# Performance work log

Hardware: AMD Instinct MI355X
Metric: run time of the kernel (lower is better)

The kernel has to match this reference:

```python
import jax, jax.numpy as jnp
import numpy as np

B, T, D_MODEL = 2, 2048, 2048
N_HEAD, N_KV, HD = 32, 8, 64


def _rope_tables(T, hd, base=10000.0):
    # standard rotary tables, (T, hd) with frequencies repeated over both halves
    inv_freq = 1.0 / (base ** (np.arange(0, hd // 2, dtype=np.float32) / (hd // 2)))
    t = np.arange(T, dtype=np.float32)
    freqs = np.outer(t, inv_freq)            # (T, hd/2)
    emb = np.concatenate([freqs, freqs], axis=-1)  # (T, hd)
    return jnp.asarray(np.cos(emb)), jnp.asarray(np.sin(emb))


def setup_inputs() -> dict:
    key = jax.random.key(0)
    ks = jax.random.split(key, 5)
    cos, sin = _rope_tables(T, HD)
    s = 0.02
    return {
        "x": jax.random.normal(ks[0], (B, T, D_MODEL), jnp.float32),
        "cos": cos,
        "sin": sin,
        "Wq": jax.random.normal(ks[1], (N_HEAD * HD, D_MODEL), jnp.float32) * s,
        "Wk": jax.random.normal(ks[2], (N_KV * HD, D_MODEL), jnp.float32) * s,
        "Wv": jax.random.normal(ks[3], (N_KV * HD, D_MODEL), jnp.float32) * s,
        "Wo": jax.random.normal(ks[4], (D_MODEL, N_HEAD * HD), jnp.float32) * s,
    }


def _apply_rope(x, cos, sin):
    # x: (B, H, T, D); cos/sin: (T, D)
    D = x.shape[-1]
    x1, x2 = x[..., : D // 2], x[..., D // 2 :]
    rot = jnp.concatenate([-x2, x1], axis=-1)
    c = cos[: x.shape[-2]][None, None]
    s = sin[: x.shape[-2]][None, None]
    return x * c + rot * s


def reference(x, cos, sin, Wq, Wk, Wv, Wo):
    Bv, Tv, _ = x.shape
    q = (x @ Wq.T).reshape(Bv, Tv, N_HEAD, HD).transpose(0, 2, 1, 3)  # (B,H,T,D)
    k = (x @ Wk.T).reshape(Bv, Tv, N_KV, HD).transpose(0, 2, 1, 3)    # (B,Hkv,T,D)
    v = (x @ Wv.T).reshape(Bv, Tv, N_KV, HD).transpose(0, 2, 1, 3)
    q = _apply_rope(q, cos, sin)
    k = _apply_rope(k, cos, sin)
    repeat = N_HEAD // N_KV
    if repeat > 1:
        k = jnp.repeat(k, repeat, axis=1)
        v = jnp.repeat(v, repeat, axis=1)
    scale = 1.0 / jnp.sqrt(jnp.float32(HD)).astype(x.dtype)
    scores = jnp.einsum("bhqd,bhkd->bhqk", q, k) * scale
    causal = jnp.tril(jnp.ones((Tv, Tv), dtype=bool))
    scores = jnp.where(causal[None, None], scores, jnp.finfo(scores.dtype).min)
    attn = jax.nn.softmax(scores, axis=-1)
    out = jnp.einsum("bhqk,bhkd->bhqd", attn, v)
    out = out.transpose(0, 2, 1, 3).reshape(Bv, Tv, N_HEAD * HD)
    return out @ Wo.T
```

## Files before the change

### kernel.cpp

```cpp
#include <hip/hip_runtime.h>
#include <stdint.h>

#define B_SZ 2
#define T_SEQ 2048
#define DM 2048
#define NH 32
#define NKV 8
#define HD 64
#define QKV_W 3072

typedef unsigned short u16;
typedef __bf16 bf16x8 __attribute__((ext_vector_type(8)));
typedef float floatx4 __attribute__((ext_vector_type(4)));

__device__ __forceinline__ float bf2f(u16 u) {
  union { unsigned u; float f; } v; v.u = ((unsigned)u) << 16; return v.f;
}
__device__ __forceinline__ u16 f2bf(float f) {
  union { float f; unsigned u; } v; v.f = f;
  unsigned r = v.u + 0x7fff + ((v.u >> 16) & 1);
  return (u16)(r >> 16);
}
__device__ __forceinline__ unsigned pk2bf(float hi, float lo) {
  return __builtin_amdgcn_perm(__float_as_uint(hi), __float_as_uint(lo), 0x07060302u);
}
__device__ __forceinline__ float fexp2(float x) {
#if __has_builtin(__builtin_amdgcn_exp2f)
  return __builtin_amdgcn_exp2f(x);
#else
  return exp2f(x);
#endif
}

__device__ __forceinline__ void gld_lds16(const void* g, void* l) {
  __builtin_amdgcn_global_load_lds(
      (const __attribute__((address_space(1))) unsigned int*)g,
      (__attribute__((address_space(3))) unsigned int*)l, 16, 0, 0);
}

__global__ __launch_bounds__(256) void conv_kernel(
    const float* __restrict__ src, u16* __restrict__ dst, int n4)
{
  int i = blockIdx.x * 256 + threadIdx.x;
  int stride = gridDim.x * 256;
  for (; i < n4; i += stride) {
    float4 v = ((const float4*)src)[i];
    ushort4 o;
    o.x = f2bf(v.x); o.y = f2bf(v.y); o.z = f2bf(v.z); o.w = f2bf(v.w);
    ((ushort4*)dst)[i] = o;
  }
}

__global__ __launch_bounds__(256) void gemm_qkv_kernel(
    const u16* __restrict__ A, const u16* __restrict__ Bt,
    u16* __restrict__ C)
{
  __shared__ __align__(16) u16 sA[128 * 32];
  __shared__ __align__(16) u16 sB[128 * 32];

  const int n0 = blockIdx.x * 128;
  const int m0 = blockIdx.y * 128;
  const int K = 2048;

  const int tid  = threadIdx.x;
  const int lane = tid & 63;
  const int w    = tid >> 6;
  const int wm = w >> 1, wn = w & 1;
  const int lm = lane & 15, lq = lane >> 4;

  floatx4 acc[4][4];
  #pragma unroll
  for (int i = 0; i < 4; i++)
    #pragma unroll
    for (int j = 0; j < 4; j++) { floatx4 z = {0.f,0.f,0.f,0.f}; acc[i][j] = z; }

  const int ar = tid >> 2;
  const int ac = (tid & 3) * 8;
  const u16* Ap0 = A  + (size_t)(m0 + ar) * K + ac;
  const u16* Ap1 = A  + (size_t)(m0 + 64 + ar) * K + ac;
  const u16* Bp0 = Bt + (size_t)(n0 + ar) * K + ac;
  const u16* Bp1 = Bt + (size_t)(n0 + 64 + ar) * K + ac;
  u16* sAd = sA + tid * 8;
  u16* sBd = sB + tid * 8;

  for (int k0 = 0; k0 < K; k0 += 32) {
    gld_lds16(Ap0 + k0, sAd);
    gld_lds16(Ap1 + k0, sAd + 2048);
    gld_lds16(Bp0 + k0, sBd);
    gld_lds16(Bp1 + k0, sBd + 2048);
    __syncthreads();

    bf16x8 af[4], bfr[4];
    #pragma unroll
    for (int mi = 0; mi < 4; mi++)
      af[mi] = *(const bf16x8*)(sA + (wm*64 + mi*16 + lm)*32 + lq*8);
    #pragma unroll
    for (int ni = 0; ni < 4; ni++)
      bfr[ni] = *(const bf16x8*)(sB + (wn*64 + ni*16 + lm)*32 + lq*8);

    #pragma unroll
    for (int mi = 0; mi < 4; mi++)
      #pragma unroll
      for (int ni = 0; ni < 4; ni++)
        acc[mi][ni] = __builtin_amdgcn_mfma_f32_16x16x32_bf16(
            af[mi], bfr[ni], acc[mi][ni], 0, 0, 0);
    __syncthreads();
  }

  #pragma unroll
  for (int mi = 0; mi < 4; mi++)
    #pragma unroll
    for (int ni = 0; ni < 4; ni++)
      #pragma unroll
      for (int r = 0; r < 4; r++) {
        int row = m0 + wm*64 + mi*16 + lq*4 + r;
        int col = n0 + wn*64 + ni*16 + lm;
        C[(size_t)row * QKV_W + col] = f2bf(acc[mi][ni][r]);
      }
}

__global__ __launch_bounds__(256) void gemm_out_kernel(
    const u16* __restrict__ A, const u16* __restrict__ Bt,
    float* __restrict__ C)
{
  __shared__ __align__(16) u16 sA[128 * 32];
  __shared__ __align__(16) u16 sB[128 * 32];

  const int n0 = blockIdx.x * 128;
  const int m0 = blockIdx.y * 128;
  const int K = 2048;

  const int tid  = threadIdx.x;
  const int lane = tid & 63;
  const int w    = tid >> 6;
  const int wm = w >> 1, wn = w & 1;
  const int lm = lane & 15, lq = lane >> 4;

  floatx4 acc[4][4];
  #pragma unroll
  for (int i = 0; i < 4; i++)
    #pragma unroll
    for (int j = 0; j < 4; j++) { floatx4 z = {0.f,0.f,0.f,0.f}; acc[i][j] = z; }

  const int ar = tid >> 2;
  const int ac = (tid & 3) * 8;
  const u16* Ap0 = A  + (size_t)(m0 + ar) * K + ac;
  const u16* Ap1 = A  + (size_t)(m0 + 64 + ar) * K + ac;
  const u16* Bp0 = Bt + (size_t)(n0 + ar) * K + ac;
  const u16* Bp1 = Bt + (size_t)(n0 + 64 + ar) * K + ac;
  u16* sAd = sA + tid * 8;
  u16* sBd = sB + tid * 8;

  for (int k0 = 0; k0 < K; k0 += 32) {
    gld_lds16(Ap0 + k0, sAd);
    gld_lds16(Ap1 + k0, sAd + 2048);
    gld_lds16(Bp0 + k0, sBd);
    gld_lds16(Bp1 + k0, sBd + 2048);
    __syncthreads();

    bf16x8 af[4], bfr[4];
    #pragma unroll
    for (int mi = 0; mi < 4; mi++)
      af[mi] = *(const bf16x8*)(sA + (wm*64 + mi*16 + lm)*32 + lq*8);
    #pragma unroll
    for (int ni = 0; ni < 4; ni++)
      bfr[ni] = *(const bf16x8*)(sB + (wn*64 + ni*16 + lm)*32 + lq*8);

    #pragma unroll
    for (int mi = 0; mi < 4; mi++)
      #pragma unroll
      for (int ni = 0; ni < 4; ni++)
        acc[mi][ni] = __builtin_amdgcn_mfma_f32_16x16x32_bf16(
            af[mi], bfr[ni], acc[mi][ni], 0, 0, 0);
    __syncthreads();
  }

  #pragma unroll
  for (int mi = 0; mi < 4; mi++)
    #pragma unroll
    for (int ni = 0; ni < 4; ni++)
      #pragma unroll
      for (int r = 0; r < 4; r++) {
        int row = m0 + wm*64 + mi*16 + lq*4 + r;
        int col = n0 + wn*64 + ni*16 + lm;
        C[(size_t)row * DM + col] = acc[mi][ni][r];
      }
}

#define QSCALE 0.180336880f
__global__ __launch_bounds__(256) void rope_kernel(
    const u16* __restrict__ qkv, const float* __restrict__ cosf,
    const float* __restrict__ sinf, u16* __restrict__ qb, u16* __restrict__ kb)
{
  const int bt = blockIdx.x;
  const int b = bt / T_SEQ, t = bt % T_SEQ;
  const int tid = threadIdx.x;
  const u16* row = qkv + (size_t)bt * QKV_W;

  #pragma unroll
  for (int i = 0; i < 4; i++) {
    int idx = i * 256 + tid;
    int h = idx >> 5, dp = idx & 31;
    float x1 = bf2f(row[h * 64 + dp]);
    float x2 = bf2f(row[h * 64 + dp + 32]);
    float c = cosf[t * 64 + dp];
    float s = sinf[t * 64 + dp];
    float o1 = (x1 * c - x2 * s) * QSCALE;
    float o2 = (x2 * c + x1 * s) * QSCALE;
    size_t base = ((size_t)(b * NH + h) * T_SEQ + t) * HD + dp;
    qb[base]      = f2bf(o1);
    qb[base + 32] = f2bf(o2);
  }
  {
    int idx = tid;
    int kvh = idx >> 5, dp = idx & 31;
    float x1 = bf2f(row[2048 + kvh * 64 + dp]);
    float x2 = bf2f(row[2048 + kvh * 64 + dp + 32]);
    float c = cosf[t * 64 + dp];
    float s = sinf[t * 64 + dp];
    size_t base = ((size_t)(b * NKV + kvh) * T_SEQ + t) * HD + dp;
    kb[base]      = f2bf(x1 * c - x2 * s);
    kb[base + 32] = f2bf(x2 * c + x1 * s);
  }
}

__global__ __launch_bounds__(256) void vtrans_kernel(
    const u16* __restrict__ qkv, u16* __restrict__ vbt)
{
  __shared__ u16 tile[64][66];
  const int t0  = blockIdx.x * 64;
  const int kvh = blockIdx.y;
  const int b   = blockIdx.z;
  const int tid = threadIdx.x;

  #pragma unroll
  for (int i = 0; i < 16; i++) {
    int idx = i * 256 + tid;
    int r = idx >> 6, c = idx & 63;
    tile[r][c] = qkv[(size_t)(b * T_SEQ + t0 + r) * QKV_W + 2560 + kvh * 64 + c];
  }
  __syncthreads();
  #pragma unroll
  for (int i = 0; i < 16; i++) {
    int idx = i * 256 + tid;
    int d = idx >> 6, c = idx & 63;
    vbt[((size_t)(b * NKV + kvh) * HD + d) * T_SEQ + t0 + c] = tile[c][d];
  }
}

__global__ __launch_bounds__(256, 2) void attn_kernel(
    const u16* __restrict__ qb, const u16* __restrict__ kb,
    const u16* __restrict__ vbt, u16* __restrict__ attn)
{
  __shared__ __align__(16) u16 sK[64 * 64];
  __shared__ __align__(16) u16 sV[64 * 64];
  __shared__ __align__(16) u16 sP[4][16][72];
  __shared__ float sAl[4][16];

  const int tid  = threadIdx.x;
  const int lane = tid & 63;
  const int w    = tid >> 6;

  const int l    = blockIdx.x;
  const int half = l >> 8;
  const int r_   = l & 255;
  const int qt   = half ? (31 - (r_ & 31)) : (r_ & 31);
  const int kv   = (r_ >> 5) & 7;
  const int b    = half;
  const int h    = kv * 4 + w;

  const int lm = lane & 15, lq = lane >> 4;
  const int sw = lm & 7;

  bf16x8 qf[4][2];
  {
    const u16* qhead = qb + ((size_t)(b * NH + h) * T_SEQ + qt * 64) * HD;
    #pragma unroll
    for (int nq = 0; nq < 4; nq++) {
      const u16* qrow = qhead + (size_t)(nq * 16 + lm) * HD + lq * 8;
      qf[nq][0] = *(const bf16x8*)(qrow);
      qf[nq][1] = *(const bf16x8*)(qrow + 32);
    }
  }

  floatx4 o_acc[4][4];
  #pragma unroll
  for (int i = 0; i < 4; i++)
    #pragma unroll
    for (int j = 0; j < 4; j++) { floatx4 z = {0.f,0.f,0.f,0.f}; o_acc[i][j] = z; }
  float m_run[4] = {-1e30f, -1e30f, -1e30f, -1e30f};
  float l_run[4] = {0.f, 0.f, 0.f, 0.f};

  const u16* kbase = kb  + (size_t)(b * NKV + kv) * T_SEQ * HD;
  const u16* vbase = vbt + (size_t)(b * NKV + kv) * HD * T_SEQ;

  const int p0row = tid >> 3,        p1row = (256 + tid) >> 3;
  const int p0ck  = (tid & 7) ^ (p0row & 7), p1ck = ((256 + tid) & 7) ^ (p1row & 7);
  const u16* kp0 = kbase + (size_t)p0row * HD + p0ck * 8;
  const u16* kp1 = kbase + (size_t)p1row * HD + p1ck * 8;
  const u16* vp0 = vbase + (size_t)p0row * T_SEQ + p0ck * 8;
  const u16* vp1 = vbase + (size_t)p1row * T_SEQ + p1ck * 8;
  char* sKd0 = (char*)sK + tid * 16;        char* sKd1 = (char*)sK + (256 + tid) * 16;
  char* sVd0 = (char*)sV + tid * 16;        char* sVd1 = (char*)sV + (256 + tid) * 16;

  for (int kt = 0; kt <= qt; kt++) {
    __syncthreads();
    gld_lds16(kp0 + (size_t)kt * 64 * HD, sKd0);
    gld_lds16(kp1 + (size_t)kt * 64 * HD, sKd1);
    gld_lds16(vp0 + kt * 64, sVd0);
    gld_lds16(vp1 + kt * 64, sVd1);
    __syncthreads();

    bf16x8 kf[4][2], vf[4][2];
    #pragma unroll
    for (int nt = 0; nt < 4; nt++) {
      kf[nt][0] = *(const bf16x8*)(sK + (((nt*16 + lm) * 8 + (lq ^ sw)) << 3));
      kf[nt][1] = *(const bf16x8*)(sK + (((nt*16 + lm) * 8 + ((4 + lq) ^ sw)) << 3));
      vf[nt][0] = *(const bf16x8*)(sV + (((nt*16 + lm) * 8 + (lq ^ sw)) << 3));
      vf[nt][1] = *(const bf16x8*)(sV + (((nt*16 + lm) * 8 + ((4 + lq) ^ sw)) << 3));
    }

    #pragma unroll
    for (int nq = 0; nq < 4; nq++) {
      floatx4 s_acc[4];
      #pragma unroll
      for (int nt = 0; nt < 4; nt++) {
        floatx4 z = {0.f,0.f,0.f,0.f};
        z = __builtin_amdgcn_mfma_f32_16x16x32_bf16(kf[nt][0], qf[nq][0], z, 0, 0, 0);
        z = __builtin_amdgcn_mfma_f32_16x16x32_bf16(kf[nt][1], qf[nq][1], z, 0, 0, 0);
        s_acc[nt] = z;
      }

      if (kt == qt) {
        #pragma unroll
        for (int nt = 0; nt < 4; nt++)
          #pragma unroll
          for (int r = 0; r < 4; r++)
            if (nt * 16 + lq * 4 + r > nq * 16 + lm) s_acc[nt][r] = -1e30f;
      }

      float mloc = s_acc[0][0];
      #pragma unroll
      for (int nt = 0; nt < 4; nt++)
        #pragma unroll
        for (int r = 0; r < 4; r++) mloc = fmaxf(mloc, s_acc[nt][r]);
      mloc = fmaxf(mloc, __shfl_xor(mloc, 16));
      mloc = fmaxf(mloc, __shfl_xor(mloc, 32));
      float mnew = fmaxf(m_run[nq], mloc);
      float al = fexp2(m_run[nq] - mnew);

      float rs = 0.f;
      uint2 pk[4];
      #pragma unroll
      for (int nt = 0; nt < 4; nt++) {
        float p0 = fexp2(s_acc[nt][0] - mnew);
        float p1 = fexp2(s_acc[nt][1] - mnew);
        float p2 = fexp2(s_acc[nt][2] - mnew);
        float p3 = fexp2(s_acc[nt][3] - mnew);
        rs += (p0 + p1) + (p2 + p3);
        pk[nt].x = pk2bf(p1, p0);
        pk[nt].y = pk2bf(p3, p2);
      }
      rs += __shfl_xor(rs, 16);
      rs += __shfl_xor(rs, 32);
      l_run[nq] = l_run[nq] * al + rs;
      m_run[nq] = mnew;

      #pragma unroll
      for (int nt = 0; nt < 4; nt++)
        *(uint2*)&sP[w][lm][nt * 16 + lq * 4] = pk[nt];

      if (lq == 0) sAl[w][lm] = al;
      floatx4 alv = *(const floatx4*)&sAl[w][lq * 4];
      #pragma unroll
      for (int nd = 0; nd < 4; nd++)
        #pragma unroll
        for (int r = 0; r < 4; r++)
          o_acc[nq][nd][r] *= alv[r];

      #pragma unroll
      for (int st = 0; st < 2; st++) {
        bf16x8 pf = *(const bf16x8*)(&sP[w][lm][st * 32 + lq * 8]);
        #pragma unroll
        for (int nd = 0; nd < 4; nd++)
          o_acc[nq][nd] = __builtin_amdgcn_mfma_f32_16x16x32_bf16(
              pf, vf[nd][st], o_acc[nq][nd], 0, 0, 0);
      }
    }
  }

  #pragma unroll
  for (int nq = 0; nq < 4; nq++) {
    __builtin_amdgcn_s_waitcnt(0);
    if (lq == 0) sAl[w][lm] = l_run[nq];
    floatx4 lv = *(const floatx4*)&sAl[w][lq * 4];
    #pragma unroll
    for (int nd = 0; nd < 4; nd++)
      #pragma unroll
      for (int r = 0; r < 4; r++) {
        float v = o_acc[nq][nd][r] / lv[r];
        size_t row = (size_t)b * T_SEQ + qt * 64 + nq * 16 + lq * 4 + r;
        attn[row * DM + h * HD + nd * 16 + lm] = f2bf(v);
      }
  }
}

extern "C" void kernel_launch(void* const* d_in, const int* in_sizes, int n_in,
                              void* d_out, int out_size, void* d_ws, size_t ws_size,
                              hipStream_t stream)
{
  const float* x    = (const float*)d_in[0];
  const float* cosf = (const float*)d_in[1];
  const float* sinf = (const float*)d_in[2];
  const float* Wq   = (const float*)d_in[3];
  const float* Wk   = (const float*)d_in[4];
  const float* Wv   = (const float*)d_in[5];
  const float* Wo   = (const float*)d_in[6];
  float* out = (float*)d_out;

  char* ws = (char*)d_ws;
  u16* qkvb  = (u16*)(ws + 0);
  u16* attnb = (u16*)(ws + 0);
  u16* qb    = (u16*)(ws + 25165824);
  u16* kb    = (u16*)(ws + 41943040);
  u16* vbt   = (u16*)(ws + 46137344);
  u16* xb    = (u16*)(ws + 50331648);
  u16* wob   = (u16*)(ws + 50331648);
  u16* wqkvb = (u16*)(ws + 67108864);

  dim3 blk(256);
  conv_kernel<<<dim3(2048), blk, 0, stream>>>(x,  xb,                 8388608 / 4);
  conv_kernel<<<dim3(1024), blk, 0, stream>>>(Wq, wqkvb,              4194304 / 4);
  conv_kernel<<<dim3(512),  blk, 0, stream>>>(Wk, wqkvb + 2048*2048,  1048576 / 4);
  conv_kernel<<<dim3(512),  blk, 0, stream>>>(Wv, wqkvb + 2560*2048,  1048576 / 4);

  gemm_qkv_kernel<<<dim3(24, 32), blk, 0, stream>>>(xb, wqkvb, qkvb);

  conv_kernel<<<dim3(1024), blk, 0, stream>>>(Wo, wob, 4194304 / 4);

  rope_kernel<<<dim3(B_SZ * T_SEQ), blk, 0, stream>>>(qkvb, cosf, sinf, qb, kb);
  vtrans_kernel<<<dim3(T_SEQ / 64, NKV, B_SZ), blk, 0, stream>>>(qkvb, vbt);
  attn_kernel<<<dim3(512), blk, 0, stream>>>(qb, kb, vbt, attnb);
  gemm_out_kernel<<<dim3(16, 32), blk, 0, stream>>>(attnb, wob, out);
}
```

Baseline: 341.3 us.

## Double-buffer attention K/V tiles, halve query tile, fuse conversion kernels

The attention kernel now uses 32-row query tiles over 1024 blocks with a new interleaved causal schedule. It double-buffers K/V tiles in LDS so the next tile's global-to-LDS load overlaps compute, and replaces LDS broadcasts of alpha and l with lane shuffles and a reciprocal multiply. The four input fp32-to-bf16 conversion launches are merged into one kernel. Together these aim to hide load latency, raise occupancy and parallelism, and cut launch overhead, at the cost of more LDS per block and K/V tiles being reloaded for twice as many blocks.

```diff
diff --git a/kernel.cpp b/kernel.cpp
--- a/kernel.cpp
+++ b/kernel.cpp
@@ -31,11 +31,43 @@
   return exp2f(x);
 #endif
 }
+__device__ __forceinline__ float frcp(float x) {
+#if __has_builtin(__builtin_amdgcn_rcpf)
+  return __builtin_amdgcn_rcpf(x);
+#else
+  return 1.0f / x;
+#endif
+}
 
 __device__ __forceinline__ void gld_lds16(const void* g, void* l) {
   __builtin_amdgcn_global_load_lds(
       (const __attribute__((address_space(1))) unsigned int*)g,
       (__attribute__((address_space(3))) unsigned int*)l, 16, 0, 0);
+}
+
+__global__ __launch_bounds__(256) void conv4_kernel(
+    const float* __restrict__ x, const float* __restrict__ wq,
+    const float* __restrict__ wk, const float* __restrict__ wv,
+    u16* __restrict__ xb, u16* __restrict__ wqkvb)
+{
+  const int N4 = 2097152 + 1048576 + 262144 + 262144;
+  ushort4* xb4 = (ushort4*)xb;
+  ushort4* wq4 = (ushort4*)wqkvb;
+  ushort4* wk4 = (ushort4*)(wqkvb + 2048 * 2048);
+  ushort4* wv4 = (ushort4*)(wqkvb + 2560 * 2048);
+  int i = blockIdx.x * 256 + threadIdx.x;
+  int stride = gridDim.x * 256;
+  for (; i < N4; i += stride) {
+    const float4* sp; ushort4* dp; int off;
+    if (i < 2097152)      { sp = (const float4*)x;  dp = xb4; off = i; }
+    else if (i < 3145728) { sp = (const float4*)wq; dp = wq4; off = i - 2097152; }
+    else if (i < 3407872) { sp = (const float4*)wk; dp = wk4; off = i - 3145728; }
+    else                  { sp = (const float4*)wv; dp = wv4; off = i - 3407872; }
+    float4 v = sp[off];
+    ushort4 o;
+    o.x = f2bf(v.x); o.y = f2bf(v.y); o.z = f2bf(v.z); o.w = f2bf(v.w);
+    dp[off] = o;
+  }
 }
 
 __global__ __launch_bounds__(256) void conv_kernel(
@@ -248,80 +280,89 @@
   }
 }
 
-__global__ __launch_bounds__(256, 2) void attn_kernel(
+__global__ __launch_bounds__(256, 3) void attn_kernel(
     const u16* __restrict__ qb, const u16* __restrict__ kb,
     const u16* __restrict__ vbt, u16* __restrict__ attn)
 {
-  __shared__ __align__(16) u16 sK[64 * 64];
-  __shared__ __align__(16) u16 sV[64 * 64];
-  __shared__ __align__(16) u16 sP[4][16][72];
-  __shared__ float sAl[4][16];
+  __shared__ __align__(16) u16 sK[2][64 * 64];
+  __shared__ __align__(16) u16 sV[2][64 * 64];
+  __shared__ __align__(16) u16 sP[4][2][16][72];
 
   const int tid  = threadIdx.x;
   const int lane = tid & 63;
   const int w    = tid >> 6;
 
-  const int l    = blockIdx.x;
-  const int half = l >> 8;
-  const int r_   = l & 255;
-  const int qt   = half ? (31 - (r_ & 31)) : (r_ & 31);
-  const int kv   = (r_ >> 5) & 7;
-  const int b    = half;
-  const int h    = kv * 4 + w;
+  const int l   = blockIdx.x;
+  const int b   = l >> 9;
+  const int m_  = l & 511;
+  const int kv  = m_ & 7;
+  const int j   = m_ >> 3;
+  const int qt2 = (j & 1) ? (63 - (j >> 1)) : (j >> 1);
+  const int h   = kv * 4 + w;
+  const int nkt = (qt2 >> 1) + 1;
 
   const int lm = lane & 15, lq = lane >> 4;
   const int sw = lm & 7;
 
-  bf16x8 qf[4][2];
+  bf16x8 qf[2][2];
   {
-    const u16* qhead = qb + ((size_t)(b * NH + h) * T_SEQ + qt * 64) * HD;
-    #pragma unroll
-    for (int nq = 0; nq < 4; nq++) {
+    const u16* qhead = qb + ((size_t)(b * NH + h) * T_SEQ + qt2 * 32) * HD;
+    #pragma unroll
+    for (int nq = 0; nq < 2; nq++) {
       const u16* qrow = qhead + (size_t)(nq * 16 + lm) * HD + lq * 8;
       qf[nq][0] = *(const bf16x8*)(qrow);
       qf[nq][1] = *(const bf16x8*)(qrow + 32);
     }
   }
 
-  floatx4 o_acc[4][4];
-  #pragma unroll
-  for (int i = 0; i < 4; i++)
-    #pragma unroll
-    for (int j = 0; j < 4; j++) { floatx4 z = {0.f,0.f,0.f,0.f}; o_acc[i][j] = z; }
-  float m_run[4] = {-1e30f, -1e30f, -1e30f, -1e30f};
-  float l_run[4] = {0.f, 0.f, 0.f, 0.f};
+  floatx4 o_acc[2][4];
+  #pragma unroll
+  for (int i = 0; i < 2; i++)
+    #pragma unroll
+    for (int jj = 0; jj < 4; jj++) { floatx4 z = {0.f,0.f,0.f,0.f}; o_acc[i][jj] = z; }
+  float m_run[2] = {-1e30f, -1e30f};
+  float l_run[2] = {0.f, 0.f};
 
   const u16* kbase = kb  + (size_t)(b * NKV + kv) * T_SEQ * HD;
-  const u16* vbase = vbt + (size_t)(b * NKV + kv) * HD * T_SEQ;
-
-  const int p0row = tid >> 3,        p1row = (256 + tid) >> 3;
-  const int p0ck  = (tid & 7) ^ (p0row & 7), p1ck = ((256 + tid) & 7) ^ (p1row & 7);
+  const u16* vbt_  = vbt + (size_t)(b * NKV + kv) * HD * T_SEQ;
+
+  const int p0row = tid >> 3,                 p1row = 32 + (tid >> 3);
+  const int p0ck  = (tid & 7) ^ (p0row & 7),  p1ck  = (tid & 7) ^ (p1row & 7);
   const u16* kp0 = kbase + (size_t)p0row * HD + p0ck * 8;
   const u16* kp1 = kbase + (size_t)p1row * HD + p1ck * 8;
-  const u16* vp0 = vbase + (size_t)p0row * T_SEQ + p0ck * 8;
-  const u16* vp1 = vbase + (size_t)p1row * T_SEQ + p1ck * 8;
-  char* sKd0 = (char*)sK + tid * 16;        char* sKd1 = (char*)sK + (256 + tid) * 16;
-  char* sVd0 = (char*)sV + tid * 16;        char* sVd1 = (char*)sV + (256 + tid) * 16;
-
-  for (int kt = 0; kt <= qt; kt++) {
+  const u16* vp0 = vbt_ + (size_t)p0row * T_SEQ + p0ck * 8;
+  const u16* vp1 = vbt_ + (size_t)p1row * T_SEQ + p1ck * 8;
+  const int d0 = tid * 16, d1 = (256 + tid) * 16;
+
+  gld_lds16(kp0, (char*)sK[0] + d0);
+  gld_lds16(kp1, (char*)sK[0] + d1);
+  gld_lds16(vp0, (char*)sV[0] + d0);
+  gld_lds16(vp1, (char*)sV[0] + d1);
+
+  for (int kt = 0; kt < nkt; kt++) {
     __syncthreads();
-    gld_lds16(kp0 + (size_t)kt * 64 * HD, sKd0);
-    gld_lds16(kp1 + (size_t)kt * 64 * HD, sKd1);
-    gld_lds16(vp0 + kt * 64, sVd0);
-    gld_lds16(vp1 + kt * 64, sVd1);
-    __syncthreads();
-
-    bf16x8 kf[4][2], vf[4][2];
+    const int cur = kt & 1;
+    if (kt + 1 < nkt) {
+      const size_t ko = (size_t)(kt + 1) * 64 * HD;
+      const int    vo = (kt + 1) * 64;
+      gld_lds16(kp0 + ko, (char*)sK[1 - cur] + d0);
+      gld_lds16(kp1 + ko, (char*)sK[1 - cur] + d1);
+      gld_lds16(vp0 + vo, (char*)sV[1 - cur] + d0);
+      gld_lds16(vp1 + vo, (char*)sV[1 - cur] + d1);
+    }
+    const u16* K = sK[cur];
+    const u16* V = sV[cur];
+    const bool last = (kt == nkt - 1);
+
+    bf16x8 kf[4][2];
     #pragma unroll
     for (int nt = 0; nt < 4; nt++) {
-      kf[nt][0] = *(const bf16x8*)(sK + (((nt*16 + lm) * 8 + (lq ^ sw)) << 3));
-      kf[nt][1] = *(const bf16x8*)(sK + (((nt*16 + lm) * 8 + ((4 + lq) ^ sw)) << 3));
-      vf[nt][0] = *(const bf16x8*)(sV + (((nt*16 + lm) * 8 + (lq ^ sw)) << 3));
-      vf[nt][1] = *(const bf16x8*)(sV + (((nt*16 + lm) * 8 + ((4 + lq) ^ sw)) << 3));
-    }
-
-    #pragma unroll
-    for (int nq = 0; nq < 4; nq++) {
+      kf[nt][0] = *(const bf16x8*)(K + (((nt*16 + lm) * 8 + (lq ^ sw)) << 3));
+      kf[nt][1] = *(const bf16x8*)(K + (((nt*16 + lm) * 8 + ((4 + lq) ^ sw)) << 3));
+    }
+
+    #pragma unroll
+    for (int nq = 0; nq < 2; nq++) {
       floatx4 s_acc[4];
       #pragma unroll
       for (int nt = 0; nt < 4; nt++) {
@@ -331,19 +372,20 @@
         s_acc[nt] = z;
       }
 
-      if (kt == qt) {
+      if (last) {
         #pragma unroll
         for (int nt = 0; nt < 4; nt++)
           #pragma unroll
           for (int r = 0; r < 4; r++)
-            if (nt * 16 + lq * 4 + r > nq * 16 + lm) s_acc[nt][r] = -1e30f;
-      }
-
-      float mloc = s_acc[0][0];
-      #pragma unroll
-      for (int nt = 0; nt < 4; nt++)
-        #pragma unroll
-        for (int r = 0; r < 4; r++) mloc = fmaxf(mloc, s_acc[nt][r]);
+            if (kt * 64 + nt * 16 + lq * 4 + r > qt2 * 32 + nq * 16 + lm)
+              s_acc[nt][r] = -1e30f;
+      }
+
+      float m01 = fmaxf(fmaxf(s_acc[0][0], s_acc[0][1]), fmaxf(s_acc[0][2], s_acc[0][3]));
+      float m23 = fmaxf(fmaxf(s_acc[1][0], s_acc[1][1]), fmaxf(s_acc[1][2], s_acc[1][3]));
+      float m45 = fmaxf(fmaxf(s_acc[2][0], s_acc[2][1]), fmaxf(s_acc[2][2], s_acc[2][3]));
+      float m67 = fmaxf(fmaxf(s_acc[3][0], s_acc[3][1]), fmaxf(s_acc[3][2], s_acc[3][3]));
+      float mloc = fmaxf(fmaxf(m01, m23), fmaxf(m45, m67));
       mloc = fmaxf(mloc, __shfl_xor(mloc, 16));
       mloc = fmaxf(mloc, __shfl_xor(mloc, 32));
       float mnew = fmaxf(m_run[nq], mloc);
@@ -368,40 +410,46 @@
 
       #pragma unroll
       for (int nt = 0; nt < 4; nt++)
-        *(uint2*)&sP[w][lm][nt * 16 + lq * 4] = pk[nt];
-
-      if (lq == 0) sAl[w][lm] = al;
-      floatx4 alv = *(const floatx4*)&sAl[w][lq * 4];
-      #pragma unroll
-      for (int nd = 0; nd < 4; nd++)
+        *(uint2*)&sP[w][nq][lm][nt * 16 + lq * 4] = pk[nt];
+
+      #pragma unroll
+      for (int r = 0; r < 4; r++) {
+        float ar_ = __shfl(al, 4 * lq + r);
         #pragma unroll
-        for (int r = 0; r < 4; r++)
-          o_acc[nq][nd][r] *= alv[r];
-
+        for (int nd = 0; nd < 4; nd++)
+          o_acc[nq][nd][r] *= ar_;
+      }
+    }
+
+    bf16x8 vf[4][2];
+    #pragma unroll
+    for (int nd = 0; nd < 4; nd++) {
+      vf[nd][0] = *(const bf16x8*)(V + (((nd*16 + lm) * 8 + (lq ^ sw)) << 3));
+      vf[nd][1] = *(const bf16x8*)(V + (((nd*16 + lm) * 8 + ((4 + lq) ^ sw)) << 3));
+    }
+    #pragma unroll
+    for (int nq = 0; nq < 2; nq++)
       #pragma unroll
       for (int st = 0; st < 2; st++) {
-        bf16x8 pf = *(const bf16x8*)(&sP[w][lm][st * 32 + lq * 8]);
+        bf16x8 pf = *(const bf16x8*)(&sP[w][nq][lm][st * 32 + lq * 8]);
         #pragma unroll
         for (int nd = 0; nd < 4; nd++)
           o_acc[nq][nd] = __builtin_amdgcn_mfma_f32_16x16x32_bf16(
               pf, vf[nd][st], o_acc[nq][nd], 0, 0, 0);
       }
-    }
-  }
-
-  #pragma unroll
-  for (int nq = 0; nq < 4; nq++) {
-    __builtin_amdgcn_s_waitcnt(0);
-    if (lq == 0) sAl[w][lm] = l_run[nq];
-    floatx4 lv = *(const floatx4*)&sAl[w][lq * 4];
-    #pragma unroll
-    for (int nd = 0; nd < 4; nd++)
-      #pragma unroll
-      for (int r = 0; r < 4; r++) {
-        float v = o_acc[nq][nd][r] / lv[r];
-        size_t row = (size_t)b * T_SEQ + qt * 64 + nq * 16 + lq * 4 + r;
-        attn[row * DM + h * HD + nd * 16 + lm] = f2bf(v);
-      }
+  }
+
+  #pragma unroll
+  for (int nq = 0; nq < 2; nq++) {
+    #pragma unroll
+    for (int r = 0; r < 4; r++) {
+      float lr = __shfl(l_run[nq], 4 * lq + r);
+      float ri = frcp(lr);
+      size_t row = (size_t)b * T_SEQ + qt2 * 32 + nq * 16 + lq * 4 + r;
+      #pragma unroll
+      for (int nd = 0; nd < 4; nd++)
+        attn[row * DM + h * HD + nd * 16 + lm] = f2bf(o_acc[nq][nd][r] * ri);
+    }
   }
 }
 
@@ -429,10 +477,7 @@
   u16* wqkvb = (u16*)(ws + 67108864);
 
   dim3 blk(256);
-  conv_kernel<<<dim3(2048), blk, 0, stream>>>(x,  xb,                 8388608 / 4);
-  conv_kernel<<<dim3(1024), blk, 0, stream>>>(Wq, wqkvb,              4194304 / 4);
-  conv_kernel<<<dim3(512),  blk, 0, stream>>>(Wk, wqkvb + 2048*2048,  1048576 / 4);
-  conv_kernel<<<dim3(512),  blk, 0, stream>>>(Wv, wqkvb + 2560*2048,  1048576 / 4);
+  conv4_kernel<<<dim3(2048), blk, 0, stream>>>(x, Wq, Wk, Wv, xb, wqkvb);
 
   gemm_qkv_kernel<<<dim3(24, 32), blk, 0, stream>>>(xb, wqkvb, qkvb);
 
@@ -440,6 +485,6 @@
 
   rope_kernel<<<dim3(B_SZ * T_SEQ), blk, 0, stream>>>(qkvb, cosf, sinf, qb, kb);
   vtrans_kernel<<<dim3(T_SEQ / 64, NKV, B_SZ), blk, 0, stream>>>(qkvb, vbt);
-  attn_kernel<<<dim3(512), blk, 0, stream>>>(qb, kb, vbt, attnb);
+  attn_kernel<<<dim3(1024), blk, 0, stream>>>(qb, kb, vbt, attnb);
   gemm_out_kernel<<<dim3(16, 32), blk, 0, stream>>>(attnb, wob, out);
 }
```

Result: no change. 342.4 us (+0.3%).
